# Optimization experiments

Measured on AMD Instinct MI355X. Metric: run time of the kernel, lower is better.

The kernel has to match this reference:

```python
import jax, jax.numpy as jnp
import numpy as np

B = 131072
# join branch layer dims: 203 -> 175 -> 150 -> 128 -> 80 -> 48
DIMS = [203, 175, 150, 128, 80, 48]

def setup_inputs() -> dict:
    key = jax.random.key(0)
    ks = jax.random.split(key, 11)
    inp = {"x": jax.random.normal(ks[0], (B, DIMS[0]), dtype=jnp.float32)}
    for i in range(5):
        fan_in, fan_out = DIMS[i], DIMS[i + 1]
        bound = 1.0 / np.sqrt(fan_in)
        inp[f"W{i+1}"] = jax.random.uniform(ks[1 + 2 * i], (fan_out, fan_in), minval=-bound, maxval=bound, dtype=jnp.float32)
        inp[f"b{i+1}"] = jax.random.uniform(ks[2 + 2 * i], (fan_out,), minval=-bound, maxval=bound, dtype=jnp.float32)
    return inp

def reference(x, W1, b1, W2, b2, W3, b3, W4, b4, W5, b5):
    # join branch of NodeEmbedding, dropout in eval mode (identity).
    h = jnp.tanh(x @ W1.T + b1)      # [B,175]
    h = jnp.tanh(h @ W2.T + b2)      # [B,150]
    h = jnp.tanh(h @ W3.T + b3)      # [B,128]
    h = jnp.tanh(h @ W4.T + b4)      # [B,80]
    return h @ W5.T + b5             # [B,48], no activation on last layer
```

## Files before the change

### kernel.cpp

```cpp
#include <hip/hip_runtime.h>


typedef short short8 __attribute__((ext_vector_type(8)));
typedef float f32x16 __attribute__((ext_vector_type(16)));
typedef unsigned int uint;
typedef unsigned short ushort;

#define PSTR 108
#define NTHREADS 384
#define MROWS 32
#define BIAS_OFF (207 * 2048)

__device__ __forceinline__ ushort f2bf(float f) {
    uint u = __float_as_uint(f);
    u += 0x7FFFu + ((u >> 16) & 1u);
    return (ushort)(u >> 16);
}
__device__ __forceinline__ float bf2f(ushort h) { return __uint_as_float(((uint)h) << 16); }
__device__ __forceinline__ float fast_tanh(float x) {
    float e = __expf(2.0f * x);
    float t = __builtin_amdgcn_rcpf(e + 1.0f);
    return fmaf(-2.0f, t, 1.0f);
}
__device__ __forceinline__ uint cvt_pk_bf16(float s0, float s1) {
    uint r;
    asm("v_cvt_pk_bf16_f32 %0, %1, %2" : "=v"(r) : "v"(s0), "v"(s1));
    return r;
}

union U4S8 { uint4 u; short8 s; };

__global__ void prep_weights(const float* __restrict__ W1, const float* __restrict__ W2,
                             const float* __restrict__ W3, const float* __restrict__ W4,
                             const float* __restrict__ W5,
                             const float* __restrict__ b1, const float* __restrict__ b2,
                             const float* __restrict__ b3, const float* __restrict__ b4,
                             const float* __restrict__ b5, char* __restrict__ ws)
{
    const int b = blockIdx.x, l = threadIdx.x;
    const int FOa[5]  = {175, 150, 128, 80, 48};
    if (b == 207) {
        float* bp = (float*)(ws + BIAS_OFF);
        const float* bs[5] = {b1, b2, b3, b4, b5};
        for (int i = l; i < 5 * 192; i += 64) {
            int L = i / 192, j = i - L * 192;
            bp[i] = (j < FOa[L]) ? bs[L][j] : 0.0f;
        }
        return;
    }
    int layer, local;
    if      (b <  78) { layer = 0; local = b; }
    else if (b < 133) { layer = 1; local = b - 78; }
    else if (b < 173) { layer = 2; local = b - 133; }
    else if (b < 197) { layer = 3; local = b - 173; }
    else              { layer = 4; local = b - 197; }
    const int NTa[5]  = {6, 5, 4, 3, 2};
    const int FINa[5] = {203, 175, 150, 128, 80};
    const float* Wp = (layer == 0) ? W1 : (layer == 1) ? W2 : (layer == 2) ? W3
                    : (layer == 3) ? W4 : W5;
    const int nt = NTa[layer], fin = FINa[layer], fout = FOa[layer];
    const int c = local / nt, t = local % nt;
    const int n  = t * 32 + (l & 31);
    const int kb = c * 16 + (l >> 5) * 8;
    uint hw[4], lw[4];
#pragma unroll
    for (int j = 0; j < 8; ++j) {
        int k = kb + j;
        float v = (n < fout && k < fin) ? Wp[(size_t)n * fin + k] : 0.0f;
        ushort hh = f2bf(v);
        ushort ll = f2bf(v - bf2f(hh));
        if (j & 1) { hw[j >> 1] |= ((uint)hh) << 16; lw[j >> 1] |= ((uint)ll) << 16; }
        else       { hw[j >> 1]  = hh;               lw[j >> 1]  = ll; }
    }
    char* dst = ws + (size_t)b * 2048 + l * 16;
    *(uint4*)dst          = make_uint4(hw[0], hw[1], hw[2], hw[3]);
    *(uint4*)(dst + 1024) = make_uint4(lw[0], lw[1], lw[2], lw[3]);
}

template<int KC, int NT, bool ACT, bool LAST>
__device__ __forceinline__ void run_layer(const char* __restrict__ wsL,
    const float* __restrict__ biasP, uint* aH, uint* aL, float* outg,
    int row0, int l, int t, int lx, int lh)
{
    f32x16 acc;
    if (t < NT) {
        const float4* bp = (const float4*)(biasP + t * 32 + 4 * lh);
#pragma unroll
        for (int q = 0; q < 4; ++q) {
            float4 bv = bp[q * 2];
            acc[4 * q + 0] = bv.x; acc[4 * q + 1] = bv.y;
            acc[4 * q + 2] = bv.z; acc[4 * q + 3] = bv.w;
        }
        const char* ha = (const char*)aH + lx * (PSTR * 4) + lh * 16;
        const char* la = (const char*)aL + lx * (PSTR * 4) + lh * 16;
        const uint4* wsb = (const uint4*)wsL + (size_t)(t * 2) * 64 + l;
#pragma unroll
        for (int c = 0; c < KC; ++c) {
            U4S8 wh, wl, ah, al;
            wh.u = wsb[(size_t)c * NT * 128];
            wl.u = wsb[(size_t)c * NT * 128 + 64];
            ah.u = *(const uint4*)(ha + c * 32);
            al.u = *(const uint4*)(la + c * 32);
            acc = __builtin_amdgcn_mfma_f32_32x32x16_bf16(wh.s, ah.s, acc, 0, 0, 0);
            acc = __builtin_amdgcn_mfma_f32_32x32x16_bf16(wh.s, al.s, acc, 0, 0, 0);
            acc = __builtin_amdgcn_mfma_f32_32x32x16_bf16(wl.s, ah.s, acc, 0, 0, 0);
        }
    }
    if (!LAST) __syncthreads();

    if (t < NT) {
        if (LAST) {
#pragma unroll
            for (int q = 0; q < 4; ++q) {
                const int f = t * 32 + 8 * q + 4 * lh;
                if (f + 3 < 48) {
                    float4 v = make_float4(acc[4 * q], acc[4 * q + 1],
                                           acc[4 * q + 2], acc[4 * q + 3]);
                    *(float4*)(outg + (size_t)(row0 + lx) * 48 + f) = v;
                }
            }
        } else {
            uint* pHd = aH + lx * PSTR;
            uint* pLd = aL + lx * PSTR;
#pragma unroll
            for (int q = 0; q < 4; ++q) {
                float t0 = acc[4 * q], t1 = acc[4 * q + 1];
                float t2 = acc[4 * q + 2], t3 = acc[4 * q + 3];
                if (ACT) { t0 = fast_tanh(t0); t1 = fast_tanh(t1);
                           t2 = fast_tanh(t2); t3 = fast_tanh(t3); }
                uint h01 = cvt_pk_bf16(t0, t1);
                uint h23 = cvt_pk_bf16(t2, t3);
                float r0 = t0 - __uint_as_float(h01 << 16);
                float r1 = t1 - __uint_as_float(h01 & 0xFFFF0000u);
                float r2 = t2 - __uint_as_float(h23 << 16);
                float r3 = t3 - __uint_as_float(h23 & 0xFFFF0000u);
                uint l01 = cvt_pk_bf16(r0, r1);
                uint l23 = cvt_pk_bf16(r2, r3);
                const int dcol = t * 16 + 4 * q + 2 * lh;
                *(uint2*)(pHd + dcol) = make_uint2(h01, h23);
                *(uint2*)(pLd + dcol) = make_uint2(l01, l23);
            }
        }
    }
    if (!LAST) __syncthreads();
}

__global__ __launch_bounds__(NTHREADS, 5)
void mlp_mfma(const float* __restrict__ x,
              const char* __restrict__ ws, float* __restrict__ out)
{
    __shared__ __align__(16) uint aH[MROWS * PSTR];
    __shared__ __align__(16) uint aL[MROWS * PSTR];

    const int tid = threadIdx.x;
    const int l = tid & 63, w = tid >> 6;
    const int lx = l & 31, lh = l >> 5;
    const int row0 = blockIdx.x * MROWS;
    const float* biasT = (const float*)(ws + BIAS_OFF);

    for (int e = tid; e < MROWS * 104; e += NTHREADS) {
        int row = e / 104, dcol = e - row * 104;
        int col = dcol * 2;
        const float* xp = x + (size_t)(row0 + row) * 203;
        float v0 = (col < 203) ? xp[col] : 0.0f;
        float v1 = (col + 1 < 203) ? xp[col + 1] : 0.0f;
        uint chi = cvt_pk_bf16(v0, v1);
        float h0 = __uint_as_float(chi << 16);
        float h1 = __uint_as_float(chi & 0xFFFF0000u);
        uint clo = cvt_pk_bf16(v0 - h0, v1 - h1);
        aH[row * PSTR + dcol] = chi;
        aL[row * PSTR + dcol] = clo;
    }
    __syncthreads();

    run_layer<13, 6, true,  false>(ws,              biasT,       aH, aL, nullptr, row0, l, w, lx, lh);
    run_layer<11, 5, true,  false>(ws +  78 * 2048, biasT + 192, aH, aL, nullptr, row0, l, w, lx, lh);
    run_layer<10, 4, true,  false>(ws + 133 * 2048, biasT + 384, aH, aL, nullptr, row0, l, w, lx, lh);
    run_layer< 8, 3, true,  false>(ws + 173 * 2048, biasT + 576, aH, aL, nullptr, row0, l, w, lx, lh);
    run_layer< 5, 2, false, true >(ws + 197 * 2048, biasT + 768, aH, aL, out,     row0, l, w, lx, lh);
}

extern "C" void kernel_launch(void* const* d_in, const int* in_sizes, int n_in,
                              void* d_out, int out_size, void* d_ws, size_t ws_size,
                              hipStream_t stream) {
    (void)in_sizes; (void)n_in; (void)ws_size; (void)out_size;
    const float* x  = (const float*)d_in[0];
    const float* W1 = (const float*)d_in[1];
    const float* b1 = (const float*)d_in[2];
    const float* W2 = (const float*)d_in[3];
    const float* b2 = (const float*)d_in[4];
    const float* W3 = (const float*)d_in[5];
    const float* b3 = (const float*)d_in[6];
    const float* W4 = (const float*)d_in[7];
    const float* b4 = (const float*)d_in[8];
    const float* W5 = (const float*)d_in[9];
    const float* b5 = (const float*)d_in[10];
    float* out = (float*)d_out;
    char* ws = (char*)d_ws;

    hipLaunchKernelGGL(prep_weights, dim3(208), dim3(64), 0, stream,
                       W1, W2, W3, W4, W5, b1, b2, b3, b4, b5, ws);
    hipLaunchKernelGGL(mlp_mfma, dim3(131072 / MROWS), dim3(NTHREADS), 0, stream,
                       x, ws, out);
}
```

Measured before the change: 286.4 us.

## Process 64 rows per block with two accumulators to reuse weight fragments

Doubles the rows per workgroup from 32 to 64. Each wave now keeps two MFMA accumulators covering two 32-row halves, so each weight fragment loaded from global memory is used twice and half as many blocks are launched. This cuts weight traffic and barrier count per row. In exchange, LDS per block doubles and register pressure rises, so the occupancy hint is lowered from 5 to 4 blocks.

```diff
diff --git a/kernel.cpp b/kernel.cpp
--- a/kernel.cpp
+++ b/kernel.cpp
@@ -8,7 +8,7 @@
 
 #define PSTR 108
 #define NTHREADS 384
-#define MROWS 32
+#define MROWS 64
 #define BIAS_OFF (207 * 2048)
 
 __device__ __forceinline__ ushort f2bf(float f) {
@@ -82,28 +82,36 @@
     const float* __restrict__ biasP, uint* aH, uint* aL, float* outg,
     int row0, int l, int t, int lx, int lh)
 {
-    f32x16 acc;
+    f32x16 accA, accB;
     if (t < NT) {
         const float4* bp = (const float4*)(biasP + t * 32 + 4 * lh);
 #pragma unroll
         for (int q = 0; q < 4; ++q) {
             float4 bv = bp[q * 2];
-            acc[4 * q + 0] = bv.x; acc[4 * q + 1] = bv.y;
-            acc[4 * q + 2] = bv.z; acc[4 * q + 3] = bv.w;
-        }
-        const char* ha = (const char*)aH + lx * (PSTR * 4) + lh * 16;
-        const char* la = (const char*)aL + lx * (PSTR * 4) + lh * 16;
+            accA[4 * q + 0] = bv.x; accA[4 * q + 1] = bv.y;
+            accA[4 * q + 2] = bv.z; accA[4 * q + 3] = bv.w;
+        }
+        accB = accA;
+        const char* h0 = (const char*)aH + lx * (PSTR * 4) + lh * 16;
+        const char* l0 = (const char*)aL + lx * (PSTR * 4) + lh * 16;
+        const char* h1 = h0 + 32 * (PSTR * 4);
+        const char* l1 = l0 + 32 * (PSTR * 4);
         const uint4* wsb = (const uint4*)wsL + (size_t)(t * 2) * 64 + l;
 #pragma unroll
         for (int c = 0; c < KC; ++c) {
-            U4S8 wh, wl, ah, al;
-            wh.u = wsb[(size_t)c * NT * 128];
-            wl.u = wsb[(size_t)c * NT * 128 + 64];
-            ah.u = *(const uint4*)(ha + c * 32);
-            al.u = *(const uint4*)(la + c * 32);
-            acc = __builtin_amdgcn_mfma_f32_32x32x16_bf16(wh.s, ah.s, acc, 0, 0, 0);
-            acc = __builtin_amdgcn_mfma_f32_32x32x16_bf16(wh.s, al.s, acc, 0, 0, 0);
-            acc = __builtin_amdgcn_mfma_f32_32x32x16_bf16(wl.s, ah.s, acc, 0, 0, 0);
+            U4S8 wh, wl, a0h, a0l, a1h, a1l;
+            wh.u  = wsb[(size_t)c * NT * 128];
+            wl.u  = wsb[(size_t)c * NT * 128 + 64];
+            a0h.u = *(const uint4*)(h0 + c * 32);
+            a0l.u = *(const uint4*)(l0 + c * 32);
+            a1h.u = *(const uint4*)(h1 + c * 32);
+            a1l.u = *(const uint4*)(l1 + c * 32);
+            accA = __builtin_amdgcn_mfma_f32_32x32x16_bf16(wh.s, a0h.s, accA, 0, 0, 0);
+            accB = __builtin_amdgcn_mfma_f32_32x32x16_bf16(wh.s, a1h.s, accB, 0, 0, 0);
+            accA = __builtin_amdgcn_mfma_f32_32x32x16_bf16(wh.s, a0l.s, accA, 0, 0, 0);
+            accB = __builtin_amdgcn_mfma_f32_32x32x16_bf16(wh.s, a1l.s, accB, 0, 0, 0);
+            accA = __builtin_amdgcn_mfma_f32_32x32x16_bf16(wl.s, a0h.s, accA, 0, 0, 0);
+            accB = __builtin_amdgcn_mfma_f32_32x32x16_bf16(wl.s, a1h.s, accB, 0, 0, 0);
         }
     }
     if (!LAST) __syncthreads();
@@ -114,38 +122,61 @@
             for (int q = 0; q < 4; ++q) {
                 const int f = t * 32 + 8 * q + 4 * lh;
                 if (f + 3 < 48) {
-                    float4 v = make_float4(acc[4 * q], acc[4 * q + 1],
-                                           acc[4 * q + 2], acc[4 * q + 3]);
-                    *(float4*)(outg + (size_t)(row0 + lx) * 48 + f) = v;
+                    float4 vA = make_float4(accA[4 * q], accA[4 * q + 1],
+                                            accA[4 * q + 2], accA[4 * q + 3]);
+                    float4 vB = make_float4(accB[4 * q], accB[4 * q + 1],
+                                            accB[4 * q + 2], accB[4 * q + 3]);
+                    *(float4*)(outg + (size_t)(row0 + lx) * 48 + f)      = vA;
+                    *(float4*)(outg + (size_t)(row0 + 32 + lx) * 48 + f) = vB;
                 }
             }
         } else {
-            uint* pHd = aH + lx * PSTR;
-            uint* pLd = aL + lx * PSTR;
+            uint* pH0 = aH + lx * PSTR;
+            uint* pL0 = aL + lx * PSTR;
+            uint* pH1 = pH0 + 32 * PSTR;
+            uint* pL1 = pL0 + 32 * PSTR;
 #pragma unroll
             for (int q = 0; q < 4; ++q) {
-                float t0 = acc[4 * q], t1 = acc[4 * q + 1];
-                float t2 = acc[4 * q + 2], t3 = acc[4 * q + 3];
-                if (ACT) { t0 = fast_tanh(t0); t1 = fast_tanh(t1);
-                           t2 = fast_tanh(t2); t3 = fast_tanh(t3); }
-                uint h01 = cvt_pk_bf16(t0, t1);
-                uint h23 = cvt_pk_bf16(t2, t3);
-                float r0 = t0 - __uint_as_float(h01 << 16);
-                float r1 = t1 - __uint_as_float(h01 & 0xFFFF0000u);
-                float r2 = t2 - __uint_as_float(h23 << 16);
-                float r3 = t3 - __uint_as_float(h23 & 0xFFFF0000u);
-                uint l01 = cvt_pk_bf16(r0, r1);
-                uint l23 = cvt_pk_bf16(r2, r3);
                 const int dcol = t * 16 + 4 * q + 2 * lh;
-                *(uint2*)(pHd + dcol) = make_uint2(h01, h23);
-                *(uint2*)(pLd + dcol) = make_uint2(l01, l23);
+                {
+                    float t0 = accA[4 * q], t1 = accA[4 * q + 1];
+                    float t2 = accA[4 * q + 2], t3 = accA[4 * q + 3];
+                    if (ACT) { t0 = fast_tanh(t0); t1 = fast_tanh(t1);
+                               t2 = fast_tanh(t2); t3 = fast_tanh(t3); }
+                    uint h01 = cvt_pk_bf16(t0, t1);
+                    uint h23 = cvt_pk_bf16(t2, t3);
+                    float r0 = t0 - __uint_as_float(h01 << 16);
+                    float r1 = t1 - __uint_as_float(h01 & 0xFFFF0000u);
+                    float r2 = t2 - __uint_as_float(h23 << 16);
+                    float r3 = t3 - __uint_as_float(h23 & 0xFFFF0000u);
+                    uint l01 = cvt_pk_bf16(r0, r1);
+                    uint l23 = cvt_pk_bf16(r2, r3);
+                    *(uint2*)(pH0 + dcol) = make_uint2(h01, h23);
+                    *(uint2*)(pL0 + dcol) = make_uint2(l01, l23);
+                }
+                {
+                    float t0 = accB[4 * q], t1 = accB[4 * q + 1];
+                    float t2 = accB[4 * q + 2], t3 = accB[4 * q + 3];
+                    if (ACT) { t0 = fast_tanh(t0); t1 = fast_tanh(t1);
+                               t2 = fast_tanh(t2); t3 = fast_tanh(t3); }
+                    uint h01 = cvt_pk_bf16(t0, t1);
+                    uint h23 = cvt_pk_bf16(t2, t3);
+                    float r0 = t0 - __uint_as_float(h01 << 16);
+                    float r1 = t1 - __uint_as_float(h01 & 0xFFFF0000u);
+                    float r2 = t2 - __uint_as_float(h23 << 16);
+                    float r3 = t3 - __uint_as_float(h23 & 0xFFFF0000u);
+                    uint l01 = cvt_pk_bf16(r0, r1);
+                    uint l23 = cvt_pk_bf16(r2, r3);
+                    *(uint2*)(pH1 + dcol) = make_uint2(h01, h23);
+                    *(uint2*)(pL1 + dcol) = make_uint2(l01, l23);
+                }
             }
         }
     }
     if (!LAST) __syncthreads();
 }
 
-__global__ __launch_bounds__(NTHREADS, 5)
+__global__ __launch_bounds__(NTHREADS, 4)
 void mlp_mfma(const float* __restrict__ x,
               const char* __restrict__ ws, float* __restrict__ out)
 {
```

Measured after the change: 361.9 us. 1.26x slower.

## Software-pipeline weight loads with inline asm and explicit vmcnt waits

Applied to the files above, without the earlier changes.

Replaces the unrolled k-loop with a compile-time recursive pipeline that issues global weight loads three chunks ahead through inline asm into a 4-slot register ring, waiting with explicit s_waitcnt vmcnt counts before each MFMA group. The goal is to hide global/L2 latency of the weight fragments behind MFMA work instead of relying on compiler scheduling. The launch bound drops from 5 to 4 waves per SIMD to give the extra buffered registers room, which lowers occupancy. The inline asm loads also bypass compiler alias tracking, so correctness depends on the manual wait counts matching the loads still in flight.

```diff
diff --git a/kernel.cpp b/kernel.cpp
--- a/kernel.cpp
+++ b/kernel.cpp
@@ -77,6 +77,34 @@
     *(uint4*)(dst + 1024) = make_uint4(lw[0], lw[1], lw[2], lw[3]);
 }
 
+template<int C, int NT>
+__device__ __forceinline__ void wissue(const uint4* wsb, U4S8* wbuf) {
+    asm volatile("global_load_dwordx4 %0, %1, off"
+                 : "=v"(wbuf[2 * (C & 3)].u)
+                 : "v"(wsb + (size_t)C * NT * 128));
+    asm volatile("global_load_dwordx4 %0, %1, off"
+                 : "=v"(wbuf[2 * (C & 3) + 1].u)
+                 : "v"(wsb + (size_t)C * NT * 128 + 64));
+}
+
+template<int C, int KC, int NT>
+__device__ __forceinline__ void kstep(const uint4* wsb, const char* ha, const char* la,
+                                      f32x16& acc, U4S8* wbuf) {
+    if constexpr (C + 3 < KC) wissue<C + 3, NT>(wsb, wbuf);
+    constexpr int PEND = (KC - C - 1) < 3 ? (KC - C - 1) : 3;
+    asm volatile("s_waitcnt vmcnt(%0)" :: "n"(2 * PEND));
+    __builtin_amdgcn_sched_barrier(0);
+    U4S8& wh = wbuf[2 * (C & 3)];
+    U4S8& wl = wbuf[2 * (C & 3) + 1];
+    U4S8 ah, al;
+    ah.u = *(const uint4*)(ha + C * 32);
+    al.u = *(const uint4*)(la + C * 32);
+    acc = __builtin_amdgcn_mfma_f32_32x32x16_bf16(wh.s, ah.s, acc, 0, 0, 0);
+    acc = __builtin_amdgcn_mfma_f32_32x32x16_bf16(wh.s, al.s, acc, 0, 0, 0);
+    acc = __builtin_amdgcn_mfma_f32_32x32x16_bf16(wl.s, ah.s, acc, 0, 0, 0);
+    if constexpr (C + 1 < KC) kstep<C + 1, KC, NT>(wsb, ha, la, acc, wbuf);
+}
+
 template<int KC, int NT, bool ACT, bool LAST>
 __device__ __forceinline__ void run_layer(const char* __restrict__ wsL,
     const float* __restrict__ biasP, uint* aH, uint* aL, float* outg,
@@ -94,17 +122,12 @@
         const char* ha = (const char*)aH + lx * (PSTR * 4) + lh * 16;
         const char* la = (const char*)aL + lx * (PSTR * 4) + lh * 16;
         const uint4* wsb = (const uint4*)wsL + (size_t)(t * 2) * 64 + l;
-#pragma unroll
-        for (int c = 0; c < KC; ++c) {
-            U4S8 wh, wl, ah, al;
-            wh.u = wsb[(size_t)c * NT * 128];
-            wl.u = wsb[(size_t)c * NT * 128 + 64];
-            ah.u = *(const uint4*)(ha + c * 32);
-            al.u = *(const uint4*)(la + c * 32);
-            acc = __builtin_amdgcn_mfma_f32_32x32x16_bf16(wh.s, ah.s, acc, 0, 0, 0);
-            acc = __builtin_amdgcn_mfma_f32_32x32x16_bf16(wh.s, al.s, acc, 0, 0, 0);
-            acc = __builtin_amdgcn_mfma_f32_32x32x16_bf16(wl.s, ah.s, acc, 0, 0, 0);
-        }
+
+        U4S8 wbuf[8];
+        wissue<0, NT>(wsb, wbuf);
+        if constexpr (KC > 1) wissue<1, NT>(wsb, wbuf);
+        if constexpr (KC > 2) wissue<2, NT>(wsb, wbuf);
+        kstep<0, KC, NT>(wsb, ha, la, acc, wbuf);
     }
     if (!LAST) __syncthreads();
 
@@ -145,7 +168,7 @@
     if (!LAST) __syncthreads();
 }
 
-__global__ __launch_bounds__(NTHREADS, 5)
+__global__ __launch_bounds__(NTHREADS, 4)
 void mlp_mfma(const float* __restrict__ x,
               const char* __restrict__ ws, float* __restrict__ out)
 {
```

After: 287.8 us. Within noise of the previous version (+0.5%).
